# Kernel tuning notes

Hardware: AMD Instinct MI355X
Metric: run time of the kernel (lower is better)

## Reference

```python
import jax, jax.numpy as jnp
import numpy as np

CH = 1024
HEADS = 8
RED = 4
PH, PW = 16, 16
DPH = max(CH // RED // HEADS, 1)   # 32
TD = DPH * HEADS                   # 256
EPS_NORM = 1e-12
EPS_BN = 1e-5


def setup_inputs() -> dict:
    key = jax.random.key(0)
    ks = jax.random.split(key, 6)
    b, h, w = 16, 64, 64
    x = jax.random.normal(ks[0], (b, CH, h, w), dtype=jnp.float32)
    # conv 1x1 weights stored as (out, in)
    w_qkv = jax.random.normal(ks[1], (3 * TD, CH), dtype=jnp.float32) * (1.0 / np.sqrt(CH))
    temperature = jnp.ones((HEADS, 1, 1), dtype=jnp.float32)
    w_proj = jax.random.normal(ks[2], (CH, TD), dtype=jnp.float32) * (1.0 / np.sqrt(TD))
    bn_gamma = jnp.ones((CH,), dtype=jnp.float32)
    bn_beta = jnp.zeros((CH,), dtype=jnp.float32)
    return {"x": x, "w_qkv": w_qkv, "temperature": temperature,
            "w_proj": w_proj, "bn_gamma": bn_gamma, "bn_beta": bn_beta}


def _l2norm(t):
    # F.normalize(dim=-1, eps=1e-12): x / max(||x||, eps)
    n = jnp.sqrt(jnp.sum(t * t, axis=-1, keepdims=True))
    return t / jnp.maximum(n, EPS_NORM)


def reference(x, w_qkv, temperature, w_proj, bn_gamma, bn_beta):
    b, c, h, w = x.shape
    # adaptive_avg_pool2d to (PH, PW); h,w divisible -> exact mean pooling
    fh, fw = h // PH, w // PW
    xr = x.reshape(b, c, PH, fh, PW, fw).mean(axis=(3, 5))          # (b,c,PH,PW)
    # 1x1 conv qkv
    qkv = jnp.einsum('ochw->ohwc', jnp.zeros((1, 1, 1, 1)))  # noop placeholder removed below
    qkv = jnp.einsum('bchw,oc->bohw', xr, w_qkv)                    # (b,3*TD,PH,PW)
    q, k, v = jnp.split(qkv, 3, axis=1)
    L = PH * PW
    def to_heads(t):
        return t.reshape(b, HEADS, DPH, L).transpose(0, 1, 3, 2)    # (b,H,L,d)
    q, k, v = to_heads(q), to_heads(k), to_heads(v)
    q = _l2norm(q)
    k = _l2norm(k)
    attn = jnp.einsum('bhld,bhmd->bhlm', q, k) * temperature        # (b,H,L,L)
    attn = jax.nn.softmax(attn, axis=-1)
    out = jnp.einsum('bhlm,bhmd->bhld', attn, v)                    # (b,H,L,d)
    out = out.transpose(0, 1, 3, 2).reshape(b, TD, PH, PW)
    # bilinear upsample, align_corners=False (half-pixel == jax 'bilinear')
    out = jax.image.resize(out, (b, TD, h, w), method='bilinear')
    # 1x1 conv projection
    out = jnp.einsum('bchw,oc->bohw', out, w_proj)                  # (b,CH,h,w)
    # BatchNorm2d in training mode: batch statistics (biased var)
    mean = out.mean(axis=(0, 2, 3), keepdims=True)
    var = out.var(axis=(0, 2, 3), keepdims=True)
    out = (out - mean) * jax.lax.rsqrt(var + EPS_BN)
    out = out * bn_gamma[None, :, None, None] + bn_beta[None, :, None, None]
    return out
```

## Files before the change

### kernel.cpp

```cpp
#include <hip/hip_runtime.h>
#include <math.h>


typedef unsigned short u16;
typedef u16 u16x8 __attribute__((ext_vector_type(8)));
typedef u16 u16x4 __attribute__((ext_vector_type(4)));
typedef short s16x8 __attribute__((ext_vector_type(8)));
typedef float f32x4 __attribute__((ext_vector_type(4)));

__device__ __forceinline__ float b2f(u16 u) {
  union { unsigned u; float f; } v;
  v.u = (unsigned)u << 16;
  return v.f;
}
__device__ __forceinline__ u16 f2b(float f) {
  union { float f; unsigned u; } v;
  v.f = f;
  unsigned r = (v.u + 0x7fffu + ((v.u >> 16) & 1u)) >> 16;
  return (u16)r;
}
__device__ __forceinline__ f32x4 mfma_bf16(s16x8 a, s16x8 b, f32x4 c) {
  return __builtin_amdgcn_mfma_f32_16x16x32_bf16(a, b, c, 0, 0, 0);
}
__device__ __forceinline__ void gload16(const u16* g, u16* l) {
  unsigned loff = (unsigned)(unsigned long long)l;
  __builtin_amdgcn_global_load_lds(
      (const __attribute__((address_space(1))) void*)g,
      (__attribute__((address_space(3))) void*)loff, 16, 0, 0);
}

__global__ __launch_bounds__(256) void cvtpool_k(
    const float* __restrict__ wa, u16* __restrict__ da, int n4a,
    const float* __restrict__ wb, u16* __restrict__ db, int n4b,
    const float* __restrict__ x, u16* __restrict__ xrN) {
  int bid = blockIdx.x;
  if (bid < 1024) {
    int idx = bid * 256 + threadIdx.x;
    const float* s;
    u16* d;
    if (idx < n4a) {
      s = wa; d = da;
    } else {
      idx -= n4a;
      if (idx >= n4b) return;
      s = wb; d = db;
    }
    f32x4 v = *((const f32x4*)s + idx);
    u16x4 o;
    o.x = f2b(v.x); o.y = f2b(v.y); o.z = f2b(v.z); o.w = f2b(v.w);
    ((u16x4*)d)[idx] = o;
    return;
  }
  bid -= 1024;
  int b = bid >> 9, i = (bid >> 5) & 15, cg = bid & 31;
  __shared__ float Ls[32][260];
  int t = threadIdx.x, lane = t & 63, wave = t >> 6;
  const float* xb = x + ((long)(b * 1024 + cg * 32)) * 4096 + i * 256;
#pragma unroll
  for (int it = 0; it < 8; ++it) {
    int cl = it * 4 + wave;
    f32x4 v = __builtin_nontemporal_load(
        (const f32x4*)(xb + (long)cl * 4096 + lane * 4));
    *(f32x4*)&Ls[cl][lane * 4] = v;
  }
  __syncthreads();
  int c = t & 31, jr = (t >> 5) & 7;
#pragma unroll
  for (int q = 0; q < 2; ++q) {
    int j = jr + q * 8;
    float s = 0.f;
#pragma unroll
    for (int r = 0; r < 4; ++r) {
      f32x4 v = *(const f32x4*)&Ls[c][r * 64 + j * 4];
      s += ((v.x + v.y) + v.z) + v.w;
    }
    xrN[((long)(b * 256 + i * 16 + j)) * 1024 + cg * 32 + c] =
        f2b(s * 0.0625f);
  }
}

template <int BM, int BN, bool OUT_BF16>
__global__ __launch_bounds__(256) void mgemm_k(const u16* __restrict__ A,
                                               const u16* __restrict__ B,
                                               void* __restrict__ C, int K,
                                               int lda, int ldb, int ldc) {
  constexpr int BK = 64;
  constexpr int FM = BM / 32, FN = BN / 32;
  __shared__ u16 As[2][BM * BK];
  __shared__ u16 Bs[2][BN * BK];
  const int t = threadIdx.x;
  const int lane = t & 63, wave = t >> 6;
  const int l15 = lane & 15, l4 = lane >> 4;
  const int row0 = blockIdx.y * BM, col0 = blockIdx.x * BN;
  const int wr = (wave >> 1) * (BM / 2), wc = (wave & 1) * (BN / 2);
  const int srow = t >> 3;
  const int sch = (t & 7) ^ (srow & 7);
  f32x4 acc[FM][FN] = {};

  auto STG = [&](int buf, int k0) {
#pragma unroll
    for (int p = 0; p < BM / 32; ++p)
      gload16(&A[(long)(row0 + p * 32 + srow) * lda + k0 + sch * 8],
              &As[buf][(p * 256 + wave * 64) * 8]);
#pragma unroll
    for (int p = 0; p < BN / 32; ++p)
      gload16(&B[(long)(col0 + p * 32 + srow) * ldb + k0 + sch * 8],
              &Bs[buf][(p * 256 + wave * 64) * 8]);
  };
  auto COMP = [&](int buf) {
#pragma unroll
    for (int kk = 0; kk < BK / 32; ++kk) {
      s16x8 a[FM], bfr[FN];
#pragma unroll
      for (int i = 0; i < FM; i++) {
        int r = wr + i * 16 + l15;
        int ph = (kk * 4 + l4) ^ (r & 7);
        a[i] = *(const s16x8*)&As[buf][r * 64 + ph * 8];
      }
#pragma unroll
      for (int j = 0; j < FN; j++) {
        int r = wc + j * 16 + l15;
        int ph = (kk * 4 + l4) ^ (r & 7);
        bfr[j] = *(const s16x8*)&Bs[buf][r * 64 + ph * 8];
      }
#pragma unroll
      for (int i = 0; i < FM; i++)
#pragma unroll
        for (int j = 0; j < FN; j++)
          acc[i][j] = mfma_bf16(a[i], bfr[j], acc[i][j]);
    }
  };

  STG(0, 0);
  __syncthreads();
  int cur = 0;
  for (int k0 = BK; k0 < K; k0 += BK) {
    STG(cur ^ 1, k0);
    COMP(cur);
    __syncthreads();
    cur ^= 1;
  }
  COMP(cur);

#pragma unroll
  for (int i = 0; i < FM; i++)
#pragma unroll
    for (int j = 0; j < FN; j++)
#pragma unroll
      for (int q = 0; q < 4; q++) {
        long r = row0 + wr + i * 16 + l4 * 4 + q;
        long c = col0 + wc + j * 16 + l15;
        if constexpr (OUT_BF16)
          ((u16*)C)[r * ldc + c] = f2b(acc[i][j][q]);
        else
          ((float*)C)[r * ldc + c] = acc[i][j][q];
      }
}

__global__ __launch_bounds__(256) void attn_k(const u16* __restrict__ qkv,
                                              const float* __restrict__ temp,
                                              u16* __restrict__ attN) {
  int blk = blockIdx.x;
  int bh = blk & 127, quar = blk >> 7;
  int b = bh >> 3, h = bh & 7;
  __shared__ u16 qs[64][40];
  __shared__ u16 ks[256][40];
  __shared__ u16 vs[32][264];
  __shared__ u16 Ps[4][16][40];
  int t = threadIdx.x, lane = t & 63, wave = t >> 6;
  int l15 = lane & 15, l4 = lane >> 4;
  long base = (long)b * 256;

  {
    const u16* V = qkv + (long)(512 + h * 32) * 4096 + base;
#pragma unroll
    for (int p = 0; p < 4; ++p) {
      int c = p * 256 + t;
      int row = c >> 5, off = (c & 31) * 8;
      *(u16x8*)&vs[row][off] = *(const u16x8*)&V[(long)row * 4096 + off];
    }
  }
  {
    const u16* Kp = qkv + (long)(256 + h * 32) * 4096 + base + t;
    float v[32], ss = 0.f;
#pragma unroll
    for (int d = 0; d < 32; ++d) {
      v[d] = b2f(Kp[(long)d * 4096]);
      ss += v[d] * v[d];
    }
    float sc = 1.f / fmaxf(sqrtf(ss), 1e-12f);
#pragma unroll
    for (int d = 0; d < 32; ++d) ks[t][d] = f2b(v[d] * sc);
  }
  if (t < 64) {
    const u16* Qp = qkv + (long)(h * 32) * 4096 + base + quar * 64 + t;
    float v[32], ss = 0.f;
#pragma unroll
    for (int d = 0; d < 32; ++d) {
      v[d] = b2f(Qp[(long)d * 4096]);
      ss += v[d] * v[d];
    }
    float sc = temp[h] / fmaxf(sqrtf(ss), 1e-12f);
#pragma unroll
    for (int d = 0; d < 32; ++d) qs[t][d] = f2b(v[d] * sc);
  }
  __syncthreads();

  int r0 = wave * 16;
  s16x8 aq = *(const s16x8*)&qs[r0 + l15][l4 * 8];
  f32x4 O[2] = {};
  float mrow[4], lrow[4];
#pragma unroll
  for (int q = 0; q < 4; ++q) {
    mrow[q] = -1e30f;
    lrow[q] = 0.f;
  }

  for (int m0 = 0; m0 < 256; m0 += 32) {
    f32x4 s[2] = {};
    s16x8 bk_[2];
#pragma unroll
    for (int j = 0; j < 2; ++j)
      bk_[j] = *(const s16x8*)&ks[m0 + j * 16 + l15][l4 * 8];
#pragma unroll
    for (int j = 0; j < 2; ++j) s[j] = mfma_bf16(aq, bk_[j], s[j]);
    float cm[4];
#pragma unroll
    for (int q = 0; q < 4; ++q) cm[q] = fmaxf(s[0][q], s[1][q]);
#pragma unroll
    for (int sh = 1; sh < 16; sh <<= 1)
#pragma unroll
      for (int q = 0; q < 4; ++q) cm[q] = fmaxf(cm[q], __shfl_xor(cm[q], sh));
    float al[4], ps[4];
#pragma unroll
    for (int q = 0; q < 4; ++q) {
      float mn = fmaxf(mrow[q], cm[q]);
      al[q] = __expf(mrow[q] - mn);
      mrow[q] = mn;
      float p0 = __expf(s[0][q] - mn);
      float p1 = __expf(s[1][q] - mn);
      s[0][q] = p0;
      s[1][q] = p1;
      ps[q] = p0 + p1;
    }
#pragma unroll
    for (int sh = 1; sh < 16; sh <<= 1)
#pragma unroll
      for (int q = 0; q < 4; ++q) ps[q] += __shfl_xor(ps[q], sh);
#pragma unroll
    for (int q = 0; q < 4; ++q) lrow[q] = lrow[q] * al[q] + ps[q];
#pragma unroll
    for (int jd = 0; jd < 2; ++jd)
#pragma unroll
      for (int q = 0; q < 4; ++q) O[jd][q] *= al[q];
#pragma unroll
    for (int j = 0; j < 2; ++j)
#pragma unroll
      for (int q = 0; q < 4; ++q)
        Ps[wave][l4 * 4 + q][j * 16 + l15] = f2b(s[j][q]);
    s16x8 pa = *(const s16x8*)&Ps[wave][l15][l4 * 8];
    s16x8 bv[2];
#pragma unroll
    for (int jd = 0; jd < 2; ++jd)
      bv[jd] = *(const s16x8*)&vs[jd * 16 + l15][m0 + l4 * 8];
#pragma unroll
    for (int jd = 0; jd < 2; ++jd) O[jd] = mfma_bf16(pa, bv[jd], O[jd]);
  }
  long rbase = base + quar * 64 + r0;
#pragma unroll
  for (int jd = 0; jd < 2; ++jd)
#pragma unroll
    for (int q = 0; q < 4; ++q)
      attN[(rbase + l4 * 4 + q) * 256 + h * 32 + jd * 16 + l15] =
          f2b(O[jd][q] / lrow[q]);
}

__global__ __launch_bounds__(256) void stats_k(const u16* __restrict__ low,
                                               const float* __restrict__ gamma,
                                               const float* __restrict__ beta,
                                               float* __restrict__ kA,
                                               float* __restrict__ kB) {
  int o = blockIdx.x, t = threadIdx.x;
  __shared__ float Lall[16][256];
  __shared__ float cw[16];
  __shared__ float A3[16][3];
  __shared__ float r1[4], r2[4];

  {
    const u16* Lp = low + (long)o * 4096;
#pragma unroll
    for (int q = 0; q < 2; ++q) {
      int idx = (q * 256 + t) * 8;
      u16x8 v = *(const u16x8*)&Lp[idx];
      int b = idx >> 8, pix = idx & 255;
#pragma unroll
      for (int e = 0; e < 8; ++e) Lall[b][pix + e] = b2f(v[e]);
    }
  }
  if (t < 16) {
    cw[t] = 0.f;
    A3[t][0] = A3[t][1] = A3[t][2] = 0.f;
  }
  __syncthreads();
  if (t < 64) {
    float src = 0.25f * t - 0.375f;
    float fl = floorf(src);
    float f = src - fl;
    int i0 = (int)fl, i1 = i0 + 1;
    i0 = max(0, min(15, i0));
    i1 = max(0, min(15, i1));
    float w0 = 1.f - f, w1 = f;
    atomicAdd(&cw[i0], w0);
    atomicAdd(&cw[i1], w1);
    if (i0 == i1)
      atomicAdd(&A3[i0][1], 1.f);
    else {
      atomicAdd(&A3[i0][1], w0 * w0);
      atomicAdd(&A3[i1][1], w1 * w1);
      atomicAdd(&A3[i0][2], w0 * w1);
      atomicAdd(&A3[i1][0], w0 * w1);
    }
  }
  __syncthreads();
  int i = t >> 4, j = t & 15;
  float s1 = 0.f, s2 = 0.f;
#pragma unroll 4
  for (int b = 0; b < 16; ++b) {
    float Lc = Lall[b][t];
    s1 += cw[i] * cw[j] * Lc;
    float a2 = 0.f;
#pragma unroll
    for (int di = -1; di <= 1; ++di) {
      int ii = max(0, min(15, i + di));
      float ay = A3[i][di + 1];
#pragma unroll
      for (int dj = -1; dj <= 1; ++dj) {
        int jj = max(0, min(15, j + dj));
        a2 += ay * A3[j][dj + 1] * Lall[b][ii * 16 + jj];
      }
    }
    s2 += a2 * Lc;
  }
  int lane = t & 63, wid = t >> 6;
  for (int off = 32; off; off >>= 1) {
    s1 += __shfl_down(s1, off);
    s2 += __shfl_down(s2, off);
  }
  if (lane == 0) {
    r1[wid] = s1;
    r2[wid] = s2;
  }
  __syncthreads();
  if (t == 0) {
    s1 = r1[0] + r1[1] + r1[2] + r1[3];
    s2 = r2[0] + r2[1] + r2[2] + r2[3];
    float mean = s1 * (1.f / 65536.f);
    float var = s2 * (1.f / 65536.f) - mean * mean;
    float is = rsqrtf(var + 1e-5f);
    float g = gamma[o];
    kA[o] = g * is;
    kB[o] = beta[o] - mean * g * is;
  }
}

__global__ __launch_bounds__(256) void up_bn_k(const u16* __restrict__ low,
                                               const float* __restrict__ kA,
                                               const float* __restrict__ kB,
                                               float* __restrict__ out) {
  long bo = blockIdx.x;
  int b = (int)(bo >> 10), o = (int)(bo & 1023);
  int t = threadIdx.x;
  __shared__ float Ls[256];
  Ls[t] = b2f(low[(long)o * 4096 + b * 256 + t]);
  __syncthreads();
  float a = kA[o], bb = kB[o];
  float* op = out + bo * 4096;
#pragma unroll
  for (int it = 0; it < 4; ++it) {
    int idx = it * 1024 + t * 4;
    int y = idx >> 6, x0 = idx & 63;
    float sy = 0.25f * y - 0.375f;
    float fly = floorf(sy);
    float fy = sy - fly;
    int y0 = max(0, min(15, (int)fly));
    int y1 = max(0, min(15, (int)fly + 1));
    const float* R0 = &Ls[y0 * 16];
    const float* R1 = &Ls[y1 * 16];
    float vout[4];
#pragma unroll
    for (int jj = 0; jj < 4; ++jj) {
      int xx = x0 + jj;
      float sx = 0.25f * xx - 0.375f;
      float flx = floorf(sx);
      float fx = sx - flx;
      int x0i = max(0, min(15, (int)flx));
      int x1i = max(0, min(15, (int)flx + 1));
      float v0 = R0[x0i] + fx * (R0[x1i] - R0[x0i]);
      float v1 = R1[x0i] + fx * (R1[x1i] - R1[x0i]);
      vout[jj] = a * (v0 + fy * (v1 - v0)) + bb;
    }
    f32x4 r;
    r.x = vout[0]; r.y = vout[1]; r.z = vout[2]; r.w = vout[3];
    __builtin_nontemporal_store(r, (f32x4*)(op + idx));
  }
}

extern "C" void kernel_launch(void* const* d_in, const int* in_sizes, int n_in,
                              void* d_out, int out_size, void* d_ws,
                              size_t ws_size, hipStream_t stream) {
  const float* x = (const float*)d_in[0];
  const float* w_qkv = (const float*)d_in[1];
  const float* temp = (const float*)d_in[2];
  const float* w_proj = (const float*)d_in[3];
  const float* gamma = (const float*)d_in[4];
  const float* beta = (const float*)d_in[5];
  float* out = (float*)d_out;
  char* w = (char*)d_ws;

  u16* wqkv_b = (u16*)(w);
  u16* wproj_b = (u16*)(w + 1572864);
  u16* xrN = (u16*)(w + 2097152);
  u16* qkvb = (u16*)(w + 10485760);
  u16* attN = (u16*)(w + 16777216);
  u16* lowB = (u16*)(w + 18874368);
  float* kA = (float*)(w + 27262976);
  float* kB = (float*)(w + 27267072);

  cvtpool_k<<<9216, 256, 0, stream>>>(w_qkv, wqkv_b, 196608, w_proj, wproj_b,
                                      65536, x, xrN);
  mgemm_k<64, 64, true><<<dim3(64, 12), 256, 0, stream>>>(
      wqkv_b, xrN, qkvb, 1024, 1024, 1024, 4096);
  attn_k<<<512, 256, 0, stream>>>(qkvb, temp, attN);
  mgemm_k<64, 64, true><<<dim3(64, 16), 256, 0, stream>>>(
      wproj_b, attN, lowB, 256, 256, 256, 4096);
  stats_k<<<1024, 256, 0, stream>>>(lowB, gamma, beta, kA, kB);
  up_bn_k<<<16384, 256, 0, stream>>>(lowB, kA, kB, out);
}
```

Measured before the change: 139.3 us.

## Split batch in halves and co-schedule pool, QKV GEMM, attention, projection stages

After: 145.1 us. +4.1%, slower.

```diff
diff --git a/kernel.cpp b/kernel.cpp
--- a/kernel.cpp
+++ b/kernel.cpp
@@ -29,31 +29,30 @@
       (__attribute__((address_space(3))) void*)loff, 16, 0, 0);
 }
 
-__global__ __launch_bounds__(256) void cvtpool_k(
-    const float* __restrict__ wa, u16* __restrict__ da, int n4a,
-    const float* __restrict__ wb, u16* __restrict__ db, int n4b,
-    const float* __restrict__ x, u16* __restrict__ xrN) {
-  int bid = blockIdx.x;
-  if (bid < 1024) {
-    int idx = bid * 256 + threadIdx.x;
-    const float* s;
-    u16* d;
-    if (idx < n4a) {
-      s = wa; d = da;
-    } else {
-      idx -= n4a;
-      if (idx >= n4b) return;
-      s = wb; d = db;
-    }
-    f32x4 v = *((const f32x4*)s + idx);
-    u16x4 o;
-    o.x = f2b(v.x); o.y = f2b(v.y); o.z = f2b(v.z); o.w = f2b(v.w);
-    ((u16x4*)d)[idx] = o;
-    return;
-  }
-  bid -= 1024;
-  int b = bid >> 9, i = (bid >> 5) & 15, cg = bid & 31;
-  __shared__ float Ls[32][260];
+__device__ __forceinline__ void dev_cvt(int bid, const float* wa, u16* da,
+                                        int n4a, const float* wb, u16* db,
+                                        int n4b) {
+  int idx = bid * 256 + threadIdx.x;
+  const float* s;
+  u16* d;
+  if (idx < n4a) {
+    s = wa; d = da;
+  } else {
+    idx -= n4a;
+    if (idx >= n4b) return;
+    s = wb; d = db;
+  }
+  f32x4 v = *((const f32x4*)s + idx);
+  u16x4 o;
+  o.x = f2b(v.x); o.y = f2b(v.y); o.z = f2b(v.z); o.w = f2b(v.w);
+  ((u16x4*)d)[idx] = o;
+}
+
+__device__ __forceinline__ void dev_pool(int bid, int b_base,
+                                         const float* __restrict__ x,
+                                         u16* __restrict__ xrN, char* smem) {
+  float(*Ls)[260] = (float(*)[260])smem;
+  int b = b_base + (bid >> 9), i = (bid >> 5) & 15, cg = bid & 31;
   int t = threadIdx.x, lane = t & 63, wave = t >> 6;
   const float* xb = x + ((long)(b * 1024 + cg * 32)) * 4096 + i * 256;
 #pragma unroll
@@ -80,34 +79,38 @@
 }
 
 template <int BM, int BN, bool OUT_BF16>
-__global__ __launch_bounds__(256) void mgemm_k(const u16* __restrict__ A,
-                                               const u16* __restrict__ B,
-                                               void* __restrict__ C, int K,
-                                               int lda, int ldb, int ldc) {
+__device__ __forceinline__ void dev_mgemm(const u16* __restrict__ A,
+                                          const u16* __restrict__ B,
+                                          void* __restrict__ C, int K, int lda,
+                                          int ldb, int ldc, int row0, int col0,
+                                          char* smem) {
   constexpr int BK = 64;
   constexpr int FM = BM / 32, FN = BN / 32;
-  __shared__ u16 As[2][BM * BK];
-  __shared__ u16 Bs[2][BN * BK];
+  u16* As0 = (u16*)smem;
+  u16* Bs0 = (u16*)smem + 2 * BM * BK;
   const int t = threadIdx.x;
   const int lane = t & 63, wave = t >> 6;
   const int l15 = lane & 15, l4 = lane >> 4;
-  const int row0 = blockIdx.y * BM, col0 = blockIdx.x * BN;
   const int wr = (wave >> 1) * (BM / 2), wc = (wave & 1) * (BN / 2);
   const int srow = t >> 3;
   const int sch = (t & 7) ^ (srow & 7);
   f32x4 acc[FM][FN] = {};
 
   auto STG = [&](int buf, int k0) {
+    u16* As = As0 + buf * BM * BK;
+    u16* Bs = Bs0 + buf * BN * BK;
 #pragma unroll
     for (int p = 0; p < BM / 32; ++p)
       gload16(&A[(long)(row0 + p * 32 + srow) * lda + k0 + sch * 8],
-              &As[buf][(p * 256 + wave * 64) * 8]);
+              &As[(p * 256 + wave * 64) * 8]);
 #pragma unroll
     for (int p = 0; p < BN / 32; ++p)
       gload16(&B[(long)(col0 + p * 32 + srow) * ldb + k0 + sch * 8],
-              &Bs[buf][(p * 256 + wave * 64) * 8]);
+              &Bs[(p * 256 + wave * 64) * 8]);
   };
   auto COMP = [&](int buf) {
+    u16* As = As0 + buf * BM * BK;
+    u16* Bs = Bs0 + buf * BN * BK;
 #pragma unroll
     for (int kk = 0; kk < BK / 32; ++kk) {
       s16x8 a[FM], bfr[FN];
@@ -115,13 +118,13 @@
       for (int i = 0; i < FM; i++) {
         int r = wr + i * 16 + l15;
         int ph = (kk * 4 + l4) ^ (r & 7);
-        a[i] = *(const s16x8*)&As[buf][r * 64 + ph * 8];
+        a[i] = *(const s16x8*)&As[r * 64 + ph * 8];
       }
 #pragma unroll
       for (int j = 0; j < FN; j++) {
         int r = wc + j * 16 + l15;
         int ph = (kk * 4 + l4) ^ (r & 7);
-        bfr[j] = *(const s16x8*)&Bs[buf][r * 64 + ph * 8];
+        bfr[j] = *(const s16x8*)&Bs[r * 64 + ph * 8];
       }
 #pragma unroll
       for (int i = 0; i < FM; i++)
@@ -157,16 +160,16 @@
       }
 }
 
-__global__ __launch_bounds__(256) void attn_k(const u16* __restrict__ qkv,
-                                              const float* __restrict__ temp,
-                                              u16* __restrict__ attN) {
-  int blk = blockIdx.x;
-  int bh = blk & 127, quar = blk >> 7;
-  int b = bh >> 3, h = bh & 7;
-  __shared__ u16 qs[64][40];
-  __shared__ u16 ks[256][40];
-  __shared__ u16 vs[32][264];
-  __shared__ u16 Ps[4][16][40];
+__device__ __forceinline__ void dev_attn(int af, int b_base,
+                                         const u16* __restrict__ qkv,
+                                         const float* __restrict__ temp,
+                                         u16* __restrict__ attN, char* smem) {
+  int bh = af & 63, quar = af >> 6;
+  int b = b_base + (bh >> 3), h = bh & 7;
+  u16(*qs)[40] = (u16(*)[40])(smem);
+  u16(*ks)[40] = (u16(*)[40])(smem + 5120);
+  u16(*vs)[264] = (u16(*)[264])(smem + 25600);
+  u16(*Ps)[16][40] = (u16(*)[16][40])(smem + 42496);
   int t = threadIdx.x, lane = t & 63, wave = t >> 6;
   int l15 = lane & 15, l4 = lane >> 4;
   long base = (long)b * 256;
@@ -273,6 +276,69 @@
     for (int q = 0; q < 4; ++q)
       attN[(rbase + l4 * 4 + q) * 256 + h * 32 + jd * 16 + l15] =
           f2b(O[jd][q] / lrow[q]);
+}
+
+__global__ __launch_bounds__(256) void k1_cvtpool(
+    const float* __restrict__ wa, u16* __restrict__ da, int n4a,
+    const float* __restrict__ wb, u16* __restrict__ db, int n4b,
+    const float* __restrict__ x, u16* __restrict__ xrN) {
+  __shared__ __align__(16) char smem[33280];
+  int bid = blockIdx.x;
+  if (bid < 1024) {
+    dev_cvt(bid, wa, da, n4a, wb, db, n4b);
+    return;
+  }
+  dev_pool(bid - 1024, 0, x, xrN, smem);
+}
+
+__global__ __launch_bounds__(256) void k2_qkv_pool(
+    const u16* __restrict__ wqkv, u16* __restrict__ xrN,
+    u16* __restrict__ qkvb, const float* __restrict__ x) {
+  __shared__ __align__(16) char smem[33280];
+  int f = blockIdx.x;
+  if (f < 384) {
+    dev_mgemm<64, 64, true>(wqkv, xrN, qkvb, 1024, 1024, 1024, 4096,
+                            (f >> 5) * 64, (f & 31) * 64, smem);
+    return;
+  }
+  dev_pool(f - 384, 8, x, xrN, smem);
+}
+
+__global__ __launch_bounds__(256) void k3_qkv_attn(
+    const u16* __restrict__ wqkv, const u16* __restrict__ xrN,
+    u16* __restrict__ qkvb, const float* __restrict__ temp,
+    u16* __restrict__ attN) {
+  __shared__ __align__(16) char smem[47616];
+  int f = blockIdx.x;
+  if (f < 384) {
+    dev_mgemm<64, 64, true>(wqkv, xrN, qkvb, 1024, 1024, 1024, 4096,
+                            (f >> 5) * 64, 2048 + (f & 31) * 64, smem);
+    return;
+  }
+  dev_attn(f - 384, 0, qkvb, temp, attN, smem);
+}
+
+__global__ __launch_bounds__(256) void k4_proj_attn(
+    const u16* __restrict__ wproj, const u16* __restrict__ attN,
+    u16* __restrict__ lowB, const u16* __restrict__ qkvb,
+    const float* __restrict__ temp, u16* __restrict__ attNw) {
+  __shared__ __align__(16) char smem[47616];
+  int f = blockIdx.x;
+  if (f < 512) {
+    dev_mgemm<64, 64, true>(wproj, attN, lowB, 256, 256, 256, 4096,
+                            (f >> 5) * 64, (f & 31) * 64, smem);
+    return;
+  }
+  dev_attn(f - 512, 8, qkvb, temp, attNw, smem);
+}
+
+__global__ __launch_bounds__(256) void k5_proj(const u16* __restrict__ wproj,
+                                               const u16* __restrict__ attN,
+                                               u16* __restrict__ lowB) {
+  __shared__ __align__(16) char smem[32768];
+  int f = blockIdx.x;
+  dev_mgemm<64, 64, true>(wproj, attN, lowB, 256, 256, 256, 4096,
+                          (f >> 5) * 64, 2048 + (f & 31) * 64, smem);
 }
 
 __global__ __launch_bounds__(256) void stats_k(const u16* __restrict__ low,
@@ -426,13 +492,12 @@
   float* kA = (float*)(w + 27262976);
   float* kB = (float*)(w + 27267072);
 
-  cvtpool_k<<<9216, 256, 0, stream>>>(w_qkv, wqkv_b, 196608, w_proj, wproj_b,
-                                      65536, x, xrN);
-  mgemm_k<64, 64, true><<<dim3(64, 12), 256, 0, stream>>>(
-      wqkv_b, xrN, qkvb, 1024, 1024, 1024, 4096);
-  attn_k<<<512, 256, 0, stream>>>(qkvb, temp, attN);
-  mgemm_k<64, 64, true><<<dim3(64, 16), 256, 0, stream>>>(
-      wproj_b, attN, lowB, 256, 256, 256, 4096);
+  k1_cvtpool<<<5120, 256, 0, stream>>>(w_qkv, wqkv_b, 196608, w_proj, wproj_b,
+                                       65536, x, xrN);
+  k2_qkv_pool<<<4480, 256, 0, stream>>>(wqkv_b, xrN, qkvb, x);
+  k3_qkv_attn<<<640, 256, 0, stream>>>(wqkv_b, xrN, qkvb, temp, attN);
+  k4_proj_attn<<<768, 256, 0, stream>>>(wproj_b, attN, lowB, qkvb, temp, attN);
+  k5_proj<<<512, 256, 0, stream>>>(wproj_b, attN, lowB);
   stats_k<<<1024, 256, 0, stream>>>(lowB, gamma, beta, kA, kB);
   up_bn_k<<<16384, 256, 0, stream>>>(lowB, kA, kB, out);
 }
```
